# Performance work log

Hardware: AMD Instinct MI355X
Metric: run time of the kernel (lower is better)

The kernel has to match this reference:

```python
import jax, jax.numpy as jnp
import numpy as np

B, T, C, H = 8, 2048, 1024, 128

def setup_inputs() -> dict:
    key = jax.random.key(0)
    k1, k2, k3, k4 = jax.random.split(key, 4)
    scale = 0.02
    return {
        "x": jax.random.normal(k1, (B, T, C), dtype=jnp.float32),
        "Wq": jax.random.normal(k2, (C, H), dtype=jnp.float32) * scale,
        "Wk": jax.random.normal(k3, (C, H), dtype=jnp.float32) * scale,
        "Wv": jax.random.normal(k4, (C, H), dtype=jnp.float32) * scale,
    }

def reference(x, Wq, Wk, Wv):
    # Single causal attention head (dropout p=0.0 -> identity)
    q = jnp.einsum('btc,ch->bth', x, Wq)
    k = jnp.einsum('btc,ch->bth', x, Wk)
    v = jnp.einsum('btc,ch->bth', x, Wv)
    head_size = k.shape[-1]
    scores = jnp.einsum('bth,bsh->bts', q, k) / jnp.sqrt(jnp.asarray(head_size, q.dtype))  # [B,T,T]
    causal = jnp.tril(jnp.ones((scores.shape[1], scores.shape[2]), dtype=bool))
    scores = jnp.where(causal, scores, -jnp.inf)
    weights = jax.nn.softmax(scores, axis=-1)
    context = jnp.einsum('bts,bsh->bth', weights, v)  # [B,T,H]
    return context
```

## Files before the change

kernel.cpp:

```cpp
#include <hip/hip_runtime.h>

typedef __bf16 bf16x8 __attribute__((ext_vector_type(8)));
typedef float f32x4 __attribute__((ext_vector_type(4)));
typedef float fv4 __attribute__((ext_vector_type(4)));

#define B_ 8
#define T_ 2048
#define C_ 1024
#define H_ 128

__device__ __forceinline__ void gload16(void* lds, const void* g) {
  __builtin_amdgcn_global_load_lds(
      (const __attribute__((address_space(1))) void*)g,
      (__attribute__((address_space(3))) void*)lds, 16, 0, 0);
}

__global__ __launch_bounds__(256) void prep_kernel(
    const float* __restrict__ Wq, const float* __restrict__ Wk,
    const float* __restrict__ Wv, __bf16* __restrict__ Wt)
{
  __shared__ __bf16 ldsT[128 * 136];
  const int tid = threadIdx.x;
  const int k0 = blockIdx.x * 128;
  const int wsel = blockIdx.y;
  const float* W = wsel == 0 ? Wq : (wsel == 1 ? Wk : Wv);
#pragma unroll
  for (int i = 0; i < 16; ++i) {
    int fidx = tid + 256 * i;
    int k = fidx >> 5, h4 = (fidx & 31) << 2;
    fv4 w = *(const fv4*)(W + (size_t)(k0 + k) * H_ + h4);
#pragma unroll
    for (int j = 0; j < 4; ++j) ldsT[(h4 + j) * 136 + k] = (__bf16)w[j];
  }
  __syncthreads();
#pragma unroll
  for (int i = 0; i < 8; ++i) {
    int sidx = tid + 256 * i;
    int h = sidx >> 4, c8 = (sidx & 15) << 3;
    *(bf16x8*)(Wt + (size_t)wsel * H_ * C_ + (size_t)h * C_ + k0 + c8) =
        *(const bf16x8*)&ldsT[h * 136 + c8];
  }
}

__global__ __launch_bounds__(256) void proj_kernel(
    const float* __restrict__ x, const __bf16* __restrict__ Wt,
    __bf16* __restrict__ Qw, __bf16* __restrict__ Kw, __bf16* __restrict__ Vtw)
{
  __shared__ __align__(16) float ldsA[2][64 * 64];
  __shared__ __align__(16) __bf16 ldsB[2][192 * 64];
  const int tid = threadIdx.x;
  const int wave = tid >> 6, lane = tid & 63;
  const int q4 = lane >> 4, l16 = lane & 15;
  const int wm = wave >> 1, wn = wave & 1;
  const int bt0 = blockIdx.x * 64;
  const int cb0 = blockIdx.y * 192;

  const int arow16 = tid >> 4, agx = tid & 15;
  const int bcol32 = tid >> 3, bgx = tid & 7;

  const f32x4 zero4 = {0.f, 0.f, 0.f, 0.f};
  f32x4 acc[2][6];
#pragma unroll
  for (int mt = 0; mt < 2; ++mt)
#pragma unroll
    for (int nt = 0; nt < 6; ++nt) acc[mt][nt] = zero4;

  auto stage = [&](int bufi, int k0) {
#pragma unroll
    for (int i = 0; i < 4; ++i) {
      int row = i * 16 + arow16;
      gload16((char*)&ldsA[bufi][0] + i * 4096 + wave * 1024,
              x + (size_t)(bt0 + row) * C_ + k0 + ((agx ^ (row & 7)) << 2));
    }
#pragma unroll
    for (int i = 0; i < 6; ++i) {
      int col = i * 32 + bcol32;
      gload16((char*)&ldsB[bufi][0] + i * 4096 + wave * 1024,
              Wt + (size_t)(cb0 + col) * C_ + k0 + ((bgx ^ (col & 7)) << 3));
    }
  };

  stage(0, 0);
  __syncthreads();

  for (int it = 0; it < 16; ++it) {
    const int buf = it & 1;
    if (it + 1 < 16) stage(buf ^ 1, (it + 1) * 64);
#pragma unroll
    for (int kc = 0; kc < 2; ++kc) {
      bf16x8 af[2];
#pragma unroll
      for (int mt = 0; mt < 2; ++mt) {
        const int rl = wm * 32 + mt * 16 + l16;
        const int rx = rl & 7;
        fv4 a0 = *(const fv4*)&ldsA[buf][rl * 64 + (((kc * 8 + q4 * 2 + 0) ^ rx) << 2)];
        fv4 a1 = *(const fv4*)&ldsA[buf][rl * 64 + (((kc * 8 + q4 * 2 + 1) ^ rx) << 2)];
#pragma unroll
        for (int j = 0; j < 4; ++j) { af[mt][j] = (__bf16)a0[j]; af[mt][4 + j] = (__bf16)a1[j]; }
      }
#pragma unroll
      for (int nt = 0; nt < 6; ++nt) {
        const int cl = wn * 96 + nt * 16 + l16;
        bf16x8 bf = *(const bf16x8*)&ldsB[buf][cl * 64 + (((kc * 4 + q4) ^ (cl & 7)) << 3)];
#pragma unroll
        for (int mt = 0; mt < 2; ++mt)
          acc[mt][nt] = __builtin_amdgcn_mfma_f32_16x16x32_bf16(af[mt], bf, acc[mt][nt], 0, 0, 0);
      }
    }
    __syncthreads();
  }

  const int b = bt0 >> 11, t0 = bt0 & (T_ - 1);
  __bf16* ldsV = (__bf16*)&ldsB[0][0];
#pragma unroll
  for (int mt = 0; mt < 2; ++mt)
#pragma unroll
    for (int nt = 0; nt < 6; ++nt) {
      int gcol = cb0 + wn * 96 + nt * 16 + l16;
#pragma unroll
      for (int r = 0; r < 4; ++r) {
        int tl = wm * 32 + mt * 16 + q4 * 4 + r;
        float v = acc[mt][nt][r];
        if (gcol < 128) Qw[(size_t)(bt0 + tl) * H_ + gcol] = (__bf16)v;
        else if (gcol < 256) Kw[(size_t)(bt0 + tl) * H_ + (gcol - 128)] = (__bf16)v;
        else ldsV[(gcol - 256) * 72 + tl] = (__bf16)v;
      }
    }
  if (cb0 == 192) {
    __syncthreads();
#pragma unroll
    for (int i = 0; i < 4; ++i) {
      int idx = tid + 256 * i;
      int h = idx >> 3, t8 = (idx & 7) << 3;
      *(bf16x8*)(Vtw + ((size_t)b * H_ + h) * T_ + t0 + t8) =
          *(const bf16x8*)&ldsV[h * 72 + t8];
    }
  }
}

__global__ __launch_bounds__(256) void attn_split(
    const __bf16* __restrict__ Q, const __bf16* __restrict__ K,
    const __bf16* __restrict__ Vt, __bf16* __restrict__ PO,
    float* __restrict__ Pl, float* __restrict__ out)
{
  __shared__ __align__(16) __bf16 ldsK[64 * 136];
  __shared__ __align__(16) __bf16 ldsV[128 * 72];
  __shared__ __align__(16) __bf16 ldsP[4][16 * 72];
  const int tid = threadIdx.x;
  const int wave = tid >> 6, lane = tid & 63;
  const int q4 = lane >> 4, l16 = lane & 15;
  const int b = blockIdx.y;
  int rem = blockIdx.x, qb = 0;
  while (rem >= (qb >> 3) + 1) { rem -= (qb >> 3) + 1; ++qb; }
  const int c = rem;
  const int tstart = c << 3;
  const int tend = min(tstart + 8, qb + 1);
  const int nch = (qb >> 3) + 1;
  const int qw = qb * 64 + wave * 16;
  const __bf16* Qb = Q + (size_t)b * T_ * H_;
  const __bf16* Kb = K + (size_t)b * T_ * H_;
  const __bf16* Vb = Vt + (size_t)b * H_ * T_;
  __bf16* ldsPw = &ldsP[wave][0];

  bf16x8 qf[4];
#pragma unroll
  for (int kc = 0; kc < 4; ++kc)
    qf[kc] = *(const bf16x8*)(Qb + (size_t)(qw + l16) * H_ + kc * 32 + q4 * 8);

  const f32x4 zero4 = {0.f, 0.f, 0.f, 0.f};
  f32x4 o[8];
#pragma unroll
  for (int nt = 0; nt < 8; ++nt) o[nt] = zero4;
  float lsum[4] = {0.f, 0.f, 0.f, 0.f};

  bf16x8 kp[4], vp[4];
#pragma unroll
  for (int i = 0; i < 4; ++i) {
    int idx = tid + 256 * i;
    int krow = idx >> 4, kcol8 = (idx & 15) << 3;
    kp[i] = *(const bf16x8*)(Kb + (size_t)(tstart * 64 + krow) * H_ + kcol8);
    int vrow = idx >> 3, vcol8 = (idx & 7) << 3;
    vp[i] = *(const bf16x8*)(Vb + (size_t)vrow * T_ + tstart * 64 + vcol8);
  }

  for (int t = tstart; t < tend; ++t) {
    const int kv0 = t << 6;
#pragma unroll
    for (int i = 0; i < 4; ++i) {
      int idx = tid + 256 * i;
      int krow = idx >> 4, kcol8 = (idx & 15) << 3;
      *(bf16x8*)&ldsK[krow * 136 + kcol8] = kp[i];
      int vrow = idx >> 3, vcol8 = (idx & 7) << 3;
      *(bf16x8*)&ldsV[vrow * 72 + vcol8] = vp[i];
    }
    __syncthreads();
    const int kvn = (t + 1 < tend) ? (kv0 + 64) : kv0;
#pragma unroll
    for (int i = 0; i < 4; ++i) {
      int idx = tid + 256 * i;
      int krow = idx >> 4, kcol8 = (idx & 15) << 3;
      kp[i] = *(const bf16x8*)(Kb + (size_t)(kvn + krow) * H_ + kcol8);
      int vrow = idx >> 3, vcol8 = (idx & 7) << 3;
      vp[i] = *(const bf16x8*)(Vb + (size_t)vrow * T_ + kvn + vcol8);
    }

    f32x4 s[4];
#pragma unroll
    for (int nt = 0; nt < 4; ++nt) s[nt] = zero4;
#pragma unroll
    for (int nt = 0; nt < 4; ++nt)
#pragma unroll
      for (int kc = 0; kc < 4; ++kc) {
        bf16x8 kf = *(const bf16x8*)&ldsK[(nt * 16 + l16) * 136 + kc * 32 + q4 * 8];
        s[nt] = __builtin_amdgcn_mfma_f32_16x16x32_bf16(qf[kc], kf, s[nt], 0, 0, 0);
      }

    if (t == qb) {
#pragma unroll
      for (int r = 0; r < 4; ++r) {
        const int grow = qw + q4 * 4 + r;
#pragma unroll
        for (int nt = 0; nt < 4; ++nt) {
          int col = kv0 + nt * 16 + l16;
          float p = (col <= grow) ? __expf(s[nt][r] * 0.08838834764831845f) : 0.f;
          lsum[r] += p;
          ldsPw[(q4 * 4 + r) * 72 + nt * 16 + l16] = (__bf16)p;
        }
      }
    } else {
#pragma unroll
      for (int r = 0; r < 4; ++r)
#pragma unroll
        for (int nt = 0; nt < 4; ++nt) {
          float p = __expf(s[nt][r] * 0.08838834764831845f);
          lsum[r] += p;
          ldsPw[(q4 * 4 + r) * 72 + nt * 16 + l16] = (__bf16)p;
        }
    }
#pragma unroll
    for (int kc2 = 0; kc2 < 2; ++kc2) {
      bf16x8 pf = *(const bf16x8*)&ldsPw[l16 * 72 + kc2 * 32 + q4 * 8];
#pragma unroll
      for (int nt = 0; nt < 8; ++nt) {
        bf16x8 vf = *(const bf16x8*)&ldsV[(nt * 16 + l16) * 72 + kc2 * 32 + q4 * 8];
        o[nt] = __builtin_amdgcn_mfma_f32_16x16x32_bf16(pf, vf, o[nt], 0, 0, 0);
      }
    }
    __syncthreads();
  }

  float lred[4];
#pragma unroll
  for (int r = 0; r < 4; ++r) {
    float l = lsum[r];
    l += __shfl_xor(l, 1);
    l += __shfl_xor(l, 2);
    l += __shfl_xor(l, 4);
    l += __shfl_xor(l, 8);
    lred[r] = l;
  }

  if (nch == 1) {
#pragma unroll
    for (int r = 0; r < 4; ++r) lred[r] = 1.f / lred[r];
#pragma unroll
    for (int nt = 0; nt < 8; ++nt)
#pragma unroll
      for (int r = 0; r < 4; ++r) {
        int row = qw + q4 * 4 + r;
        out[((size_t)b * T_ + row) * H_ + nt * 16 + l16] = o[nt][r] * lred[r];
      }
  } else {
    const int slot = b * 80 + qb + max(qb - 8, 0) + max(qb - 16, 0) + max(qb - 24, 0) + c;
    __bf16* POs = PO + (size_t)slot * 8192;
#pragma unroll
    for (int nt = 0; nt < 8; ++nt)
#pragma unroll
      for (int r = 0; r < 4; ++r)
        POs[(wave * 16 + q4 * 4 + r) * 128 + nt * 16 + l16] = (__bf16)o[nt][r];
    if (l16 == 0)
#pragma unroll
      for (int r = 0; r < 4; ++r)
        Pl[slot * 64 + wave * 16 + q4 * 4 + r] = lred[r];
  }
}

__global__ __launch_bounds__(256) void attn_combine(
    const __bf16* __restrict__ PO, const float* __restrict__ Pl,
    float* __restrict__ out)
{
  const int qb = 8 + (blockIdx.x >> 2);
  const int seg = blockIdx.x & 3;
  const int b = blockIdx.y;
  const int nch = (qb >> 3) + 1;
  const int slot0 = b * 80 + qb + max(qb - 8, 0) + max(qb - 16, 0) + max(qb - 24, 0);
  const int tid = threadIdx.x;
  const int rloc = seg * 16 + (tid >> 4);
  const int col8 = (tid & 15) << 3;
  float oacc[8] = {0.f};
  float lacc = 0.f;
  for (int cc = 0; cc < nch; ++cc) {
    const int slot = slot0 + cc;
    lacc += Pl[slot * 64 + rloc];
    bf16x8 v = *(const bf16x8*)(PO + (size_t)slot * 8192 + rloc * 128 + col8);
#pragma unroll
    for (int j = 0; j < 8; ++j) oacc[j] += (float)v[j];
  }
  const float inv = 1.f / lacc;
  float* op = out + ((size_t)b * T_ + qb * 64 + rloc) * H_ + col8;
  fv4 v0, v1;
#pragma unroll
  for (int j = 0; j < 4; ++j) { v0[j] = oacc[j] * inv; v1[j] = oacc[4 + j] * inv; }
  *(fv4*)op = v0;
  *(fv4*)(op + 4) = v1;
}

__global__ __launch_bounds__(256) void attn_mono(
    const __bf16* __restrict__ Q, const __bf16* __restrict__ K,
    const __bf16* __restrict__ Vt, float* __restrict__ out)
{
  __shared__ __align__(16) __bf16 ldsK[64 * 136];
  __shared__ __align__(16) __bf16 ldsV[128 * 72];
  __shared__ __align__(16) __bf16 ldsP[4][16 * 72];
  const int tid = threadIdx.x;
  const int wave = tid >> 6, lane = tid & 63;
  const int q4 = lane >> 4, l16 = lane & 15;
  const int qb = blockIdx.x, b = blockIdx.y;
  const int qw = qb * 64 + wave * 16;
  const __bf16* Qb = Q + (size_t)b * T_ * H_;
  const __bf16* Kb = K + (size_t)b * T_ * H_;
  const __bf16* Vb = Vt + (size_t)b * H_ * T_;
  __bf16* ldsPw = &ldsP[wave][0];

  bf16x8 qf[4];
#pragma unroll
  for (int kc = 0; kc < 4; ++kc)
    qf[kc] = *(const bf16x8*)(Qb + (size_t)(qw + l16) * H_ + kc * 32 + q4 * 8);

  const f32x4 zero4 = {0.f, 0.f, 0.f, 0.f};
  f32x4 o[8];
#pragma unroll
  for (int nt = 0; nt < 8; ++nt) o[nt] = zero4;
  float lsum[4] = {0.f, 0.f, 0.f, 0.f};
  const int ntile = qb + 1;

  bf16x8 kp[4], vp[4];
#pragma unroll
  for (int i = 0; i < 4; ++i) {
    int idx = tid + 256 * i;
    int krow = idx >> 4, kcol8 = (idx & 15) << 3;
    kp[i] = *(const bf16x8*)(Kb + (size_t)krow * H_ + kcol8);
    int vrow = idx >> 3, vcol8 = (idx & 7) << 3;
    vp[i] = *(const bf16x8*)(Vb + (size_t)vrow * T_ + vcol8);
  }

  for (int t = 0; t < ntile; ++t) {
    const int kv0 = t << 6;
#pragma unroll
    for (int i = 0; i < 4; ++i) {
      int idx = tid + 256 * i;
      int krow = idx >> 4, kcol8 = (idx & 15) << 3;
      *(bf16x8*)&ldsK[krow * 136 + kcol8] = kp[i];
      int vrow = idx >> 3, vcol8 = (idx & 7) << 3;
      *(bf16x8*)&ldsV[vrow * 72 + vcol8] = vp[i];
    }
    __syncthreads();
    int kvn = (t + 1 < ntile) ? (kv0 + 64) : kv0;
#pragma unroll
    for (int i = 0; i < 4; ++i) {
      int idx = tid + 256 * i;
      int krow = idx >> 4, kcol8 = (idx & 15) << 3;
      kp[i] = *(const bf16x8*)(Kb + (size_t)(kvn + krow) * H_ + kcol8);
      int vrow = idx >> 3, vcol8 = (idx & 7) << 3;
      vp[i] = *(const bf16x8*)(Vb + (size_t)vrow * T_ + kvn + vcol8);
    }
    f32x4 s[4];
#pragma unroll
    for (int nt = 0; nt < 4; ++nt) s[nt] = zero4;
#pragma unroll
    for (int nt = 0; nt < 4; ++nt)
#pragma unroll
      for (int kc = 0; kc < 4; ++kc) {
        bf16x8 kf = *(const bf16x8*)&ldsK[(nt * 16 + l16) * 136 + kc * 32 + q4 * 8];
        s[nt] = __builtin_amdgcn_mfma_f32_16x16x32_bf16(qf[kc], kf, s[nt], 0, 0, 0);
      }
#pragma unroll
    for (int r = 0; r < 4; ++r) {
      const int grow = qw + q4 * 4 + r;
#pragma unroll
      for (int nt = 0; nt < 4; ++nt) {
        int col = kv0 + nt * 16 + l16;
        float p = (col <= grow) ? __expf(s[nt][r] * 0.08838834764831845f) : 0.f;
        lsum[r] += p;
        ldsPw[(q4 * 4 + r) * 72 + nt * 16 + l16] = (__bf16)p;
      }
    }
#pragma unroll
    for (int kc2 = 0; kc2 < 2; ++kc2) {
      bf16x8 pf = *(const bf16x8*)&ldsPw[l16 * 72 + kc2 * 32 + q4 * 8];
#pragma unroll
      for (int nt = 0; nt < 8; ++nt) {
        bf16x8 vf = *(const bf16x8*)&ldsV[(nt * 16 + l16) * 72 + kc2 * 32 + q4 * 8];
        o[nt] = __builtin_amdgcn_mfma_f32_16x16x32_bf16(pf, vf, o[nt], 0, 0, 0);
      }
    }
    __syncthreads();
  }
  float rinv[4];
#pragma unroll
  for (int r = 0; r < 4; ++r) {
    float l = lsum[r];
    l += __shfl_xor(l, 1);
    l += __shfl_xor(l, 2);
    l += __shfl_xor(l, 4);
    l += __shfl_xor(l, 8);
    rinv[r] = 1.f / l;
  }
#pragma unroll
  for (int nt = 0; nt < 8; ++nt)
#pragma unroll
    for (int r = 0; r < 4; ++r) {
      int row = qw + q4 * 4 + r;
      out[((size_t)b * T_ + row) * H_ + nt * 16 + l16] = o[nt][r] * rinv[r];
    }
}

extern "C" void kernel_launch(void* const* d_in, const int* in_sizes, int n_in,
                              void* d_out, int out_size, void* d_ws, size_t ws_size,
                              hipStream_t stream) {
  const float* x  = (const float*)d_in[0];
  const float* Wq = (const float*)d_in[1];
  const float* Wk = (const float*)d_in[2];
  const float* Wv = (const float*)d_in[3];
  __bf16* ws = (__bf16*)d_ws;
  __bf16* Qw  = ws;
  __bf16* Kw  = ws + (size_t)B_ * T_ * H_;
  __bf16* Vtw = ws + (size_t)2 * B_ * T_ * H_;
  __bf16* Wt  = ws + (size_t)3 * B_ * T_ * H_;
  const size_t bf16_elems = 6684672;
  __bf16* PO = ws + bf16_elems;
  float* Pl = (float*)(ws + bf16_elems + (size_t)640 * 8192);
  const size_t need = bf16_elems * 2 + (size_t)640 * 8192 * 2 + (size_t)640 * 64 * 4;
  float* out = (float*)d_out;

  prep_kernel<<<dim3(8, 3), 256, 0, stream>>>(Wq, Wk, Wv, Wt);
  proj_kernel<<<dim3(256, 2), 256, 0, stream>>>(x, Wt, Qw, Kw, Vtw);
  if (ws_size >= need) {
    attn_split<<<dim3(80, 8), 256, 0, stream>>>(Qw, Kw, Vtw, PO, Pl, out);
    attn_combine<<<dim3(96, 8), 256, 0, stream>>>(PO, Pl, out);
  } else {
    attn_mono<<<dim3(32, 8), 256, 0, stream>>>(Qw, Kw, Vtw, out);
  }
}
```

Before: 157.1 us.

## Fuse split-K combine into attn_split via last-block atomic counter

Removes the separate attn_combine launch. Each split block now publishes its partial output, bumps a per-(batch, query-block) atomic counter, and the last-arriving block reduces all partials and writes the final output. The counters are zeroed in prep_kernel. This saves one kernel launch and its tail, at the cost of fences, an atomic, and a serial reduction done by a single block per query tile.

Result: slower. 261.9 us (+66.7%).

```diff
diff --git a/kernel.cpp b/kernel.cpp
--- a/kernel.cpp
+++ b/kernel.cpp
@@ -17,12 +17,13 @@
 
 __global__ __launch_bounds__(256) void prep_kernel(
     const float* __restrict__ Wq, const float* __restrict__ Wk,
-    const float* __restrict__ Wv, __bf16* __restrict__ Wt)
+    const float* __restrict__ Wv, __bf16* __restrict__ Wt, int* __restrict__ Cnt)
 {
   __shared__ __bf16 ldsT[128 * 136];
   const int tid = threadIdx.x;
   const int k0 = blockIdx.x * 128;
   const int wsel = blockIdx.y;
+  if (Cnt && blockIdx.x == 0 && blockIdx.y == 0) Cnt[tid] = 0;
   const float* W = wsel == 0 ? Wq : (wsel == 1 ? Wk : Wv);
 #pragma unroll
   for (int i = 0; i < 16; ++i) {
@@ -141,11 +142,12 @@
 __global__ __launch_bounds__(256) void attn_split(
     const __bf16* __restrict__ Q, const __bf16* __restrict__ K,
     const __bf16* __restrict__ Vt, __bf16* __restrict__ PO,
-    float* __restrict__ Pl, float* __restrict__ out)
+    float* __restrict__ Pl, int* __restrict__ Cnt, float* __restrict__ out)
 {
   __shared__ __align__(16) __bf16 ldsK[64 * 136];
   __shared__ __align__(16) __bf16 ldsV[128 * 72];
   __shared__ __align__(16) __bf16 ldsP[4][16 * 72];
+  __shared__ int sprev;
   const int tid = threadIdx.x;
   const int wave = tid >> 6, lane = tid & 63;
   const int q4 = lane >> 4, l16 = lane & 15;
@@ -271,7 +273,8 @@
         out[((size_t)b * T_ + row) * H_ + nt * 16 + l16] = o[nt][r] * lred[r];
       }
   } else {
-    const int slot = b * 80 + qb + max(qb - 8, 0) + max(qb - 16, 0) + max(qb - 24, 0) + c;
+    const int slot0 = b * 80 + qb + max(qb - 8, 0) + max(qb - 16, 0) + max(qb - 24, 0);
+    const int slot = slot0 + c;
     __bf16* POs = PO + (size_t)slot * 8192;
 #pragma unroll
     for (int nt = 0; nt < 8; ++nt)
@@ -282,37 +285,41 @@
 #pragma unroll
       for (int r = 0; r < 4; ++r)
         Pl[slot * 64 + wave * 16 + q4 * 4 + r] = lred[r];
-  }
-}
-
-__global__ __launch_bounds__(256) void attn_combine(
-    const __bf16* __restrict__ PO, const float* __restrict__ Pl,
-    float* __restrict__ out)
-{
-  const int qb = 8 + (blockIdx.x >> 2);
-  const int seg = blockIdx.x & 3;
-  const int b = blockIdx.y;
-  const int nch = (qb >> 3) + 1;
-  const int slot0 = b * 80 + qb + max(qb - 8, 0) + max(qb - 16, 0) + max(qb - 24, 0);
-  const int tid = threadIdx.x;
-  const int rloc = seg * 16 + (tid >> 4);
-  const int col8 = (tid & 15) << 3;
-  float oacc[8] = {0.f};
-  float lacc = 0.f;
-  for (int cc = 0; cc < nch; ++cc) {
-    const int slot = slot0 + cc;
-    lacc += Pl[slot * 64 + rloc];
-    bf16x8 v = *(const bf16x8*)(PO + (size_t)slot * 8192 + rloc * 128 + col8);
-#pragma unroll
-    for (int j = 0; j < 8; ++j) oacc[j] += (float)v[j];
-  }
-  const float inv = 1.f / lacc;
-  float* op = out + ((size_t)b * T_ + qb * 64 + rloc) * H_ + col8;
-  fv4 v0, v1;
-#pragma unroll
-  for (int j = 0; j < 4; ++j) { v0[j] = oacc[j] * inv; v1[j] = oacc[4 + j] * inv; }
-  *(fv4*)op = v0;
-  *(fv4*)(op + 4) = v1;
+
+    __threadfence();
+    __syncthreads();
+    if (tid == 0) sprev = atomicAdd(&Cnt[b * 32 + qb], 1);
+    __syncthreads();
+    if (sprev == nch - 1) {
+      __threadfence();
+      const int row = tid >> 2;
+      const int cs = (tid & 3) << 5;
+      float lacc = 0.f;
+      float oc[32];
+#pragma unroll
+      for (int j = 0; j < 32; ++j) oc[j] = 0.f;
+      for (int cc = 0; cc < nch; ++cc) {
+        const int s2 = slot0 + cc;
+        lacc += Pl[s2 * 64 + row];
+        const __bf16* pp = PO + (size_t)s2 * 8192 + row * 128 + cs;
+#pragma unroll
+        for (int g = 0; g < 4; ++g) {
+          bf16x8 v = *(const bf16x8*)(pp + g * 8);
+#pragma unroll
+          for (int j = 0; j < 8; ++j) oc[g * 8 + j] += (float)v[j];
+        }
+      }
+      const float inv = 1.f / lacc;
+      float* op = out + ((size_t)b * T_ + qb * 64 + row) * H_ + cs;
+#pragma unroll
+      for (int g = 0; g < 8; ++g) {
+        fv4 v;
+#pragma unroll
+        for (int j = 0; j < 4; ++j) v[j] = oc[g * 4 + j] * inv;
+        *(fv4*)(op + g * 4) = v;
+      }
+    }
+  }
 }
 
 __global__ __launch_bounds__(256) void attn_mono(
@@ -440,14 +447,15 @@
   const size_t bf16_elems = 6684672;
   __bf16* PO = ws + bf16_elems;
   float* Pl = (float*)(ws + bf16_elems + (size_t)640 * 8192);
-  const size_t need = bf16_elems * 2 + (size_t)640 * 8192 * 2 + (size_t)640 * 64 * 4;
+  int* Cnt = (int*)(Pl + 640 * 64);
+  const size_t need = bf16_elems * 2 + (size_t)640 * 8192 * 2 + (size_t)640 * 64 * 4 + 1024;
   float* out = (float*)d_out;
 
-  prep_kernel<<<dim3(8, 3), 256, 0, stream>>>(Wq, Wk, Wv, Wt);
+  const bool split = ws_size >= need;
+  prep_kernel<<<dim3(8, 3), 256, 0, stream>>>(Wq, Wk, Wv, Wt, split ? Cnt : (int*)nullptr);
   proj_kernel<<<dim3(256, 2), 256, 0, stream>>>(x, Wt, Qw, Kw, Vtw);
-  if (ws_size >= need) {
-    attn_split<<<dim3(80, 8), 256, 0, stream>>>(Qw, Kw, Vtw, PO, Pl, out);
-    attn_combine<<<dim3(96, 8), 256, 0, stream>>>(PO, Pl, out);
+  if (split) {
+    attn_split<<<dim3(80, 8), 256, 0, stream>>>(Qw, Kw, Vtw, PO, Pl, Cnt, out);
   } else {
     attn_mono<<<dim3(32, 8), 256, 0, stream>>>(Qw, Kw, Vtw, out);
   }
```

## Stage K/V tiles with direct global-to-LDS loads into double-buffered swizzled LDS

Applied to the files above, without the earlier changes.

Replaces the register-staged K/V prefetch, where tiles were loaded into registers and then written to LDS, with `global_load_lds` async copies straight into LDS. The LDS tiles are now double-buffered so the next tile is fetched while the current one is consumed. The padded LDS rows are replaced by an XOR chunk swizzle to avoid bank conflicts without padding. This removes the LDS store instructions and frees the prefetch registers. In exchange, LDS use doubles for K/V, and correctness depends on the end-of-iteration barrier waiting for the outstanding async loads.

Result: no change. 158.5 us (+0.9%).

```diff
diff --git a/kernel.cpp b/kernel.cpp
--- a/kernel.cpp
+++ b/kernel.cpp
@@ -14,6 +14,7 @@
       (const __attribute__((address_space(1))) void*)g,
       (__attribute__((address_space(3))) void*)lds, 16, 0, 0);
 }
+
 
 __global__ __launch_bounds__(256) void prep_kernel(
     const float* __restrict__ Wq, const float* __restrict__ Wk,
@@ -143,8 +144,8 @@
     const __bf16* __restrict__ Vt, __bf16* __restrict__ PO,
     float* __restrict__ Pl, float* __restrict__ out)
 {
-  __shared__ __align__(16) __bf16 ldsK[64 * 136];
-  __shared__ __align__(16) __bf16 ldsV[128 * 72];
+  __shared__ __align__(16) __bf16 ldsK[2][64 * 128];
+  __shared__ __align__(16) __bf16 ldsV[2][128 * 64];
   __shared__ __align__(16) __bf16 ldsP[4][16 * 72];
   const int tid = threadIdx.x;
   const int wave = tid >> 6, lane = tid & 63;
@@ -173,47 +174,40 @@
   for (int nt = 0; nt < 8; ++nt) o[nt] = zero4;
   float lsum[4] = {0.f, 0.f, 0.f, 0.f};
 
-  bf16x8 kp[4], vp[4];
-#pragma unroll
-  for (int i = 0; i < 4; ++i) {
-    int idx = tid + 256 * i;
-    int krow = idx >> 4, kcol8 = (idx & 15) << 3;
-    kp[i] = *(const bf16x8*)(Kb + (size_t)(tstart * 64 + krow) * H_ + kcol8);
-    int vrow = idx >> 3, vcol8 = (idx & 7) << 3;
-    vp[i] = *(const bf16x8*)(Vb + (size_t)vrow * T_ + tstart * 64 + vcol8);
-  }
+  auto stageKV = [&](int bufi, int t) {
+    const int kv0 = t << 6;
+#pragma unroll
+    for (int i = 0; i < 4; ++i) {
+      int kr = i * 16 + (tid >> 4);
+      gload16((char*)&ldsK[bufi][0] + i * 4096 + wave * 1024,
+              Kb + (size_t)(kv0 + kr) * H_ + (((tid & 15) ^ (kr & 7)) << 3));
+      int vr = i * 32 + (tid >> 3);
+      gload16((char*)&ldsV[bufi][0] + i * 4096 + wave * 1024,
+              Vb + (size_t)vr * T_ + kv0 + (((tid & 7) ^ (vr & 7)) << 3));
+    }
+  };
+
+  stageKV(0, tstart);
+  __syncthreads();
 
   for (int t = tstart; t < tend; ++t) {
+    const int buf = (t - tstart) & 1;
     const int kv0 = t << 6;
-#pragma unroll
-    for (int i = 0; i < 4; ++i) {
-      int idx = tid + 256 * i;
-      int krow = idx >> 4, kcol8 = (idx & 15) << 3;
-      *(bf16x8*)&ldsK[krow * 136 + kcol8] = kp[i];
-      int vrow = idx >> 3, vcol8 = (idx & 7) << 3;
-      *(bf16x8*)&ldsV[vrow * 72 + vcol8] = vp[i];
-    }
-    __syncthreads();
-    const int kvn = (t + 1 < tend) ? (kv0 + 64) : kv0;
-#pragma unroll
-    for (int i = 0; i < 4; ++i) {
-      int idx = tid + 256 * i;
-      int krow = idx >> 4, kcol8 = (idx & 15) << 3;
-      kp[i] = *(const bf16x8*)(Kb + (size_t)(kvn + krow) * H_ + kcol8);
-      int vrow = idx >> 3, vcol8 = (idx & 7) << 3;
-      vp[i] = *(const bf16x8*)(Vb + (size_t)vrow * T_ + kvn + vcol8);
-    }
+    if (t + 1 < tend) stageKV(buf ^ 1, t + 1);
 
     f32x4 s[4];
 #pragma unroll
     for (int nt = 0; nt < 4; ++nt) s[nt] = zero4;
 #pragma unroll
-    for (int nt = 0; nt < 4; ++nt)
+    for (int nt = 0; nt < 4; ++nt) {
+      const int krow = nt * 16 + l16;
+      const int kx = krow & 7;
 #pragma unroll
       for (int kc = 0; kc < 4; ++kc) {
-        bf16x8 kf = *(const bf16x8*)&ldsK[(nt * 16 + l16) * 136 + kc * 32 + q4 * 8];
+        bf16x8 kf = *(const bf16x8*)&ldsK[buf][krow * 128 + (((kc * 4 + q4) ^ kx) << 3)];
         s[nt] = __builtin_amdgcn_mfma_f32_16x16x32_bf16(qf[kc], kf, s[nt], 0, 0, 0);
       }
+    }
 
     if (t == qb) {
 #pragma unroll
@@ -242,7 +236,8 @@
       bf16x8 pf = *(const bf16x8*)&ldsPw[l16 * 72 + kc2 * 32 + q4 * 8];
 #pragma unroll
       for (int nt = 0; nt < 8; ++nt) {
-        bf16x8 vf = *(const bf16x8*)&ldsV[(nt * 16 + l16) * 72 + kc2 * 32 + q4 * 8];
+        const int vrow = nt * 16 + l16;
+        bf16x8 vf = *(const bf16x8*)&ldsV[buf][vrow * 64 + (((kc2 * 4 + q4) ^ (vrow & 7)) << 3)];
         o[nt] = __builtin_amdgcn_mfma_f32_16x16x32_bf16(pf, vf, o[nt], 0, 0, 0);
       }
     }
```
